# Kernel optimization log

Hardware: AMD Instinct MI355X
Metric: run time of the kernel (lower is better)

Reference implementation:

```python
import jax, jax.numpy as jnp
import numpy as np

BATCH = 1024
LATENT = 16
IMG = 3 * 96 * 96  # 27648


def setup_inputs() -> dict:
    key = jax.random.key(0)
    ks = jax.random.split(key, 16)
    w = lambda k, shape, s=0.05: (jax.random.normal(k, shape, jnp.float32) * s)
    return {
        "x": jax.random.normal(ks[0], (BATCH, 96, 96, 3), jnp.float32),
        "eps_noise": jax.random.normal(ks[1], (BATCH, LATENT), jnp.float32),
        "enc_w1": w(ks[2], (IMG, 900)),
        "enc_b1": jnp.zeros((900,), jnp.float32),
        "enc_w2": w(ks[3], (900, 300)),
        "enc_b2": jnp.zeros((300,), jnp.float32),
        "logvar_w": w(ks[4], (300, LATENT)),
        "logvar_b": jnp.zeros((LATENT,), jnp.float32),
        "W": w(ks[5], (LATENT, LATENT), 0.1),  # nn.init.normal_(std=0.1)
        "dec_w1": w(ks[6], (LATENT, 300)),
        "dec_b1": jnp.zeros((300,), jnp.float32),
        "dec_w2": w(ks[7], (300, 300)),
        "dec_b2": jnp.zeros((300,), jnp.float32),
        "dec_w3": w(ks[8], (300, IMG)),
        "dec_b3": jnp.zeros((IMG,), jnp.float32),
    }


def reference(x, eps_noise, enc_w1, enc_b1, enc_w2, enc_b2, logvar_w, logvar_b,
              W, dec_w1, dec_b1, dec_w2, dec_b2, dec_w3, dec_b3):
    # encoder
    xf = x.reshape(x.shape[0], -1)                      # [B, 27648]
    h = jax.nn.elu(xf @ enc_w1 + enc_b1)
    h = jax.nn.elu(h @ enc_w2 + enc_b2)
    logvar = h @ logvar_w + logvar_b                    # [B, d]

    d = W.shape[0]
    idx = jnp.arange(d, dtype=W.dtype)
    relu_y = jnp.maximum(idx[None, :] - idx[:, None], 0.0)  # ReLU(j - i), strictly upper tri
    Bmat = W * relu_y                                    # strictly upper triangular

    # latent generating process: z_j = sum_{i<j} z_i B[i,j] + eps_j  <=>  z (I - B) = eps
    eps = jnp.exp(logvar / 2.0) * eps_noise             # [B, d]
    A = jnp.eye(d, dtype=W.dtype) - Bmat                # upper triangular
    # solve A^T z^T = eps^T (forward substitution), one fused triangular solve
    z = jax.scipy.linalg.solve_triangular(A, eps.T, trans=1, lower=False).T
    Bz = z @ Bmat                                       # equals per-column z[:, :j] @ B[:j, j]

    # decoder
    g = jax.nn.elu(z @ dec_w1 + dec_b1)
    g = jax.nn.elu(g @ dec_w2 + dec_b2)
    xhat = jnp.tanh(g @ dec_w3 + dec_b3).reshape(-1, 96, 96, 3)
    return z, logvar, Bz, Bmat, xhat
```

## Files before the change

kernel.cpp:

```cpp
#include <hip/hip_runtime.h>
#include <math.h>

#define ACT_NONE 0
#define ACT_ELU  1
#define ACT_TANH 2

typedef unsigned short u16;
typedef unsigned int   u32;
typedef __attribute__((ext_vector_type(8))) short short8;
typedef __attribute__((ext_vector_type(4))) float f32x4;

__device__ __forceinline__ float eluf(float v) { return v > 0.f ? v : __expf(v) - 1.f; }
__device__ __forceinline__ float tanh_fast(float v) {
    float t = __expf(2.f * v);
    return 1.f - 2.f / (t + 1.f);
}
__device__ __forceinline__ u16 bf16_rne(float x) {
    u32 u = __float_as_uint(x);
    u32 r = u + 0x7FFFu + ((u >> 16) & 1u);
    return (u16)(r >> 16);
}

__global__ __launch_bounds__(256) void splitX(
    const float* __restrict__ in, u16* __restrict__ hi, u16* __restrict__ lo, int n)
{
    int i = (blockIdx.x * 256 + threadIdx.x) * 8;
    if (i >= n) return;
    float4 v0 = reinterpret_cast<const float4*>(in + i)[0];
    float4 v1 = reinterpret_cast<const float4*>(in + i)[1];
    float f[8] = {v0.x, v0.y, v0.z, v0.w, v1.x, v1.y, v1.z, v1.w};
    alignas(16) u16 h[8], l[8];
#pragma unroll
    for (int e = 0; e < 8; ++e) {
        u16 hh = bf16_rne(f[e]);
        h[e] = hh;
        float hf = __uint_as_float((u32)hh << 16);
        l[e] = bf16_rne(f[e] - hf);
    }
    *reinterpret_cast<uint4*>(hi + i) = *reinterpret_cast<uint4*>(&h[0]);
    *reinterpret_cast<uint4*>(lo + i) = *reinterpret_cast<uint4*>(&l[0]);
}

__global__ __launch_bounds__(256) void convT(
    const float* __restrict__ in, int K, int N,
    u16* __restrict__ outHi, u16* __restrict__ outLo, int ldo)
{
    __shared__ float tile[32][33];
    const int t  = threadIdx.x;
    const int kt = blockIdx.x * 32;
    const int nt = blockIdx.y * 32;
    {
        int r = t >> 3, c = (t & 7) * 4;
        int gk = kt + r;
        float4 v = {0.f, 0.f, 0.f, 0.f};
        if (gk < K) {
            const float* p = in + (size_t)gk * N + nt + c;
            if (nt + c + 3 < N) {
                v = *reinterpret_cast<const float4*>(p);
            } else {
                if (nt + c + 0 < N) v.x = p[0];
                if (nt + c + 1 < N) v.y = p[1];
                if (nt + c + 2 < N) v.z = p[2];
                if (nt + c + 3 < N) v.w = p[3];
            }
        }
        tile[r][c] = v.x; tile[r][c + 1] = v.y; tile[r][c + 2] = v.z; tile[r][c + 3] = v.w;
    }
    __syncthreads();
    {
        int r = t >> 3, c = (t & 7) * 4;
        ushort4 h, l;
        float f[4];
#pragma unroll
        for (int e = 0; e < 4; ++e) f[e] = tile[c + e][r];
        u16 hh[4], ll[4];
#pragma unroll
        for (int e = 0; e < 4; ++e) {
            hh[e] = bf16_rne(f[e]);
            float hf = __uint_as_float((u32)hh[e] << 16);
            ll[e] = bf16_rne(f[e] - hf);
        }
        h.x = hh[0]; h.y = hh[1]; h.z = hh[2]; h.w = hh[3];
        l.x = ll[0]; l.y = ll[1]; l.z = ll[2]; l.w = ll[3];
        size_t o = (size_t)(nt + r) * ldo + kt + c;
        *reinterpret_cast<ushort4*>(outHi + o) = h;
        *reinterpret_cast<ushort4*>(outLo + o) = l;
    }
}

template <int ACT, bool ATOMIC>
__global__ __launch_bounds__(256) void mgemm2(
    const u16* __restrict__ Ahi, const u16* __restrict__ Alo, int lda,
    const u16* __restrict__ Bhi, const u16* __restrict__ Blo, int ldb,
    const float* __restrict__ bias,
    float* __restrict__ C, int ldc,
    int Ncols, int kChunk, int Ktot)
{
    __shared__ u16 As[2][128][40];
    __shared__ u16 Bs[2][128][40];

    const int tid  = threadIdx.x;
    const int m0   = blockIdx.y * 128;
    const int n0   = blockIdx.x * 128;
    const int kbeg = blockIdx.z * kChunk;
    const int kend = min(Ktot, kbeg + kChunk);

    const int w  = tid >> 6;
    const int wm = (w >> 1) * 64;
    const int wn = (w & 1) * 64;
    const int ln = tid & 63;
    const int fr = ln & 15;
    const int kh = ln >> 4;

    const int srow = tid >> 1;
    const int skq  = (tid & 1) * 16;

    const u16* pAh = Ahi + (size_t)(m0 + srow) * lda + skq;
    const u16* pAl = Alo + (size_t)(m0 + srow) * lda + skq;
    const u16* pBh = Bhi + (size_t)(n0 + srow) * ldb + skq;
    const u16* pBl = Blo + (size_t)(n0 + srow) * ldb + skq;

    uint4 r0, r1, r2, r3, r4, r5, r6, r7;
#define LOADK(kk) do {                                                   \
        r0 = *reinterpret_cast<const uint4*>(pAh + (kk));                \
        r1 = *reinterpret_cast<const uint4*>(pAh + (kk) + 8);            \
        r2 = *reinterpret_cast<const uint4*>(pAl + (kk));                \
        r3 = *reinterpret_cast<const uint4*>(pAl + (kk) + 8);            \
        r4 = *reinterpret_cast<const uint4*>(pBh + (kk));                \
        r5 = *reinterpret_cast<const uint4*>(pBh + (kk) + 8);            \
        r6 = *reinterpret_cast<const uint4*>(pBl + (kk));                \
        r7 = *reinterpret_cast<const uint4*>(pBl + (kk) + 8);            \
    } while (0)

    f32x4 acc[4][4];
#pragma unroll
    for (int i = 0; i < 4; ++i)
#pragma unroll
        for (int j = 0; j < 4; ++j) {
            f32x4 z = {0.f, 0.f, 0.f, 0.f};
            acc[i][j] = z;
        }

    LOADK(kbeg);
    for (int k0 = kbeg; k0 < kend; k0 += 32) {
        *reinterpret_cast<uint4*>(&As[0][srow][skq])     = r0;
        *reinterpret_cast<uint4*>(&As[0][srow][skq + 8]) = r1;
        *reinterpret_cast<uint4*>(&As[1][srow][skq])     = r2;
        *reinterpret_cast<uint4*>(&As[1][srow][skq + 8]) = r3;
        *reinterpret_cast<uint4*>(&Bs[0][srow][skq])     = r4;
        *reinterpret_cast<uint4*>(&Bs[0][srow][skq + 8]) = r5;
        *reinterpret_cast<uint4*>(&Bs[1][srow][skq])     = r6;
        *reinterpret_cast<uint4*>(&Bs[1][srow][skq + 8]) = r7;
        __syncthreads();

        if (k0 + 32 < kend) LOADK(k0 + 32);

        short8 ah[4], al[4], bh[4], bl[4];
#pragma unroll
        for (int i = 0; i < 4; ++i) {
            ah[i] = *reinterpret_cast<const short8*>(&As[0][wm + i * 16 + fr][kh * 8]);
            al[i] = *reinterpret_cast<const short8*>(&As[1][wm + i * 16 + fr][kh * 8]);
        }
#pragma unroll
        for (int j = 0; j < 4; ++j) {
            bh[j] = *reinterpret_cast<const short8*>(&Bs[0][wn + j * 16 + fr][kh * 8]);
            bl[j] = *reinterpret_cast<const short8*>(&Bs[1][wn + j * 16 + fr][kh * 8]);
        }
#pragma unroll
        for (int i = 0; i < 4; ++i)
#pragma unroll
            for (int j = 0; j < 4; ++j) {
                acc[i][j] = __builtin_amdgcn_mfma_f32_16x16x32_bf16(ah[i], bh[j], acc[i][j], 0, 0, 0);
                acc[i][j] = __builtin_amdgcn_mfma_f32_16x16x32_bf16(ah[i], bl[j], acc[i][j], 0, 0, 0);
                acc[i][j] = __builtin_amdgcn_mfma_f32_16x16x32_bf16(al[i], bh[j], acc[i][j], 0, 0, 0);
            }
        __syncthreads();
    }
#undef LOADK

#pragma unroll
    for (int j = 0; j < 4; ++j) {
        const int col = n0 + wn + j * 16 + fr;
        float bv = 0.f;
        if (!ATOMIC) bv = bias[col];
#pragma unroll
        for (int i = 0; i < 4; ++i) {
            const int rowb = m0 + wm + i * 16 + kh * 4;
#pragma unroll
            for (int p = 0; p < 4; ++p) {
                float v = acc[i][j][p];
                const int row = rowb + p;
                if (ATOMIC) {
                    if (col < Ncols) atomicAdd(&C[(size_t)row * ldc + col], v);
                } else {
                    v += bv;
                    if (ACT == ACT_TANH) v = tanh_fast(v);
                    else if (ACT == ACT_ELU) v = eluf(v);
                    C[(size_t)row * ldc + col] = v;
                }
            }
        }
    }
}

__global__ __launch_bounds__(256) void zero_f32(float* __restrict__ p, int n)
{
    int i = blockIdx.x * 256 + threadIdx.x;
    if (i < n) p[i] = 0.f;
}

__global__ __launch_bounds__(256) void bias_elu_inplace(
    float* __restrict__ p, const float* __restrict__ bias, int n, int N)
{
    int i = blockIdx.x * 256 + threadIdx.x;
    if (i < n) p[i] = eluf(p[i] + bias[i % N]);
}

template <int ACT>
__global__ __launch_bounds__(256) void rowgemm(
    const float* __restrict__ A, int strideA,
    const float* __restrict__ W, const float* __restrict__ bias,
    float* __restrict__ out, int strideOut, int padWidth,
    int N, int K)
{
    __shared__ float Arow[928];
    const int m = blockIdx.x;
    const int t = threadIdx.x;
    for (int k = t; k < K; k += 256) Arow[k] = A[(size_t)m * strideA + k];
    __syncthreads();
    for (int n = t; n < padWidth; n += 256) {
        float s = 0.f;
        if (n < N) {
            s = bias[n];
            for (int k = 0; k < K; ++k) s = fmaf(Arow[k], W[(size_t)k * N + n], s);
            if (ACT == ACT_ELU) s = eluf(s);
        }
        out[(size_t)m * strideOut + n] = s;
    }
}

__global__ __launch_bounds__(256) void rowgemm_split(
    const float* __restrict__ A, int strideA,
    const float* __restrict__ W, const float* __restrict__ bias,
    u16* __restrict__ outHi, u16* __restrict__ outLo, int strideOut, int padWidth,
    int N, int K)
{
    __shared__ float Arow[928];
    const int m = blockIdx.x;
    const int t = threadIdx.x;
    for (int k = t; k < K; k += 256) Arow[k] = A[(size_t)m * strideA + k];
    __syncthreads();
    for (int n = t; n < padWidth; n += 256) {
        u16 hh = 0, ll = 0;
        if (n < N) {
            float s = bias[n];
            for (int k = 0; k < K; ++k) s = fmaf(Arow[k], W[(size_t)k * N + n], s);
            s = eluf(s);
            hh = bf16_rne(s);
            float hf = __uint_as_float((u32)hh << 16);
            ll = bf16_rne(s - hf);
        }
        outHi[(size_t)m * strideOut + n] = hh;
        outLo[(size_t)m * strideOut + n] = ll;
    }
}

__global__ __launch_bounds__(256) void latent_kernel(
    const float* __restrict__ logvar,
    const float* __restrict__ eps_noise,
    const float* __restrict__ Wlat,
    float* __restrict__ z_ws,
    float* __restrict__ out)
{
    __shared__ float Bm[256];
    const int t = threadIdx.x;
    {
        int i = t >> 4, j = t & 15;
        float v = (j > i) ? Wlat[t] * (float)(j - i) : 0.f;
        Bm[t] = v;
        if (blockIdx.x == 0) out[49152 + t] = v;
    }
    __syncthreads();

    const int b = blockIdx.x * 256 + t;
    float lv[16], z[16];
#pragma unroll
    for (int j = 0; j < 16; ++j) lv[j] = logvar[b * 16 + j];
#pragma unroll
    for (int j = 0; j < 16; ++j) {
        float s = __expf(0.5f * fminf(lv[j], 80.f)) * eps_noise[b * 16 + j];
        for (int i = 0; i < j; ++i) s = fmaf(z[i], Bm[i * 16 + j], s);
        z[j] = s;
    }
#pragma unroll
    for (int j = 0; j < 16; ++j) {
        float bz = 0.f;
#pragma unroll
        for (int i = 0; i < 16; ++i) bz = fmaf(z[i], Bm[i * 16 + j], bz);
        out[b * 16 + j]         = z[j];
        out[16384 + b * 16 + j] = lv[j];
        out[32768 + b * 16 + j] = bz;
        z_ws[b * 16 + j] = z[j];
    }
}

extern "C" void kernel_launch(void* const* d_in, const int* in_sizes, int n_in,
                              void* d_out, int out_size, void* d_ws, size_t ws_size,
                              hipStream_t stream)
{
    const float* x       = (const float*)d_in[0];
    const float* eps_n   = (const float*)d_in[1];
    const float* enc_w1  = (const float*)d_in[2];
    const float* enc_b1  = (const float*)d_in[3];
    const float* enc_w2  = (const float*)d_in[4];
    const float* enc_b2  = (const float*)d_in[5];
    const float* lv_w    = (const float*)d_in[6];
    const float* lv_b    = (const float*)d_in[7];
    const float* Wlat    = (const float*)d_in[8];
    const float* dec_w1  = (const float*)d_in[9];
    const float* dec_b1  = (const float*)d_in[10];
    const float* dec_w2  = (const float*)d_in[11];
    const float* dec_b2  = (const float*)d_in[12];
    const float* dec_w3  = (const float*)d_in[13];
    const float* dec_b3  = (const float*)d_in[14];

    char* ws = (char*)d_ws;
    float* h1     = (float*)(ws + 0);
    float* h2     = (float*)(ws + 3686400);
    float* lv     = (float*)(ws + 4915200);
    float* zf     = (float*)(ws + 4980736);
    float* g1     = (float*)(ws + 5046272);
    u16*   g2hi   = (u16*)(ws + 6275072);
    u16*   g2lo   = (u16*)(ws + 6930432);
    u16*   xhi    = (u16*)(ws + 7585792);
    u16*   xlo    = (u16*)(ws + 64208896);
    u16*   w1t_hi = (u16*)(ws + 120832000);
    u16*   w1t_lo = (u16*)(ws + 177455104);
    u16*   w3t_hi = (u16*)(ws + 234078208);
    u16*   w3t_lo = (u16*)(ws + 251772928);

    float* out = (float*)d_out;

    splitX<<<13824, 256, 0, stream>>>(x, xhi, xlo, 28311552);

    convT<<<dim3(864, 32), 256, 0, stream>>>(enc_w1, 27648, 900, w1t_hi, w1t_lo, 27648);
    convT<<<dim3(10, 864), 256, 0, stream>>>(dec_w3, 300, 27648, w3t_hi, w3t_lo, 320);

    zero_f32<<<3600, 256, 0, stream>>>(h1, 921600);

    mgemm2<ACT_NONE, true><<<dim3(8, 8, 16), 256, 0, stream>>>(
        xhi, xlo, 27648, w1t_hi, w1t_lo, 27648, nullptr,
        h1, 900, 900, 1728, 27648);

    bias_elu_inplace<<<3600, 256, 0, stream>>>(h1, enc_b1, 921600, 900);

    rowgemm<ACT_ELU><<<1024, 256, 0, stream>>>(
        h1, 900, enc_w2, enc_b2, h2, 300, 300, 300, 900);

    rowgemm<ACT_NONE><<<1024, 256, 0, stream>>>(
        h2, 300, lv_w, lv_b, lv, 16, 16, 16, 300);

    latent_kernel<<<4, 256, 0, stream>>>(lv, eps_n, Wlat, zf, out);

    rowgemm<ACT_ELU><<<1024, 256, 0, stream>>>(
        zf, 16, dec_w1, dec_b1, g1, 300, 300, 300, 16);

    rowgemm_split<<<1024, 256, 0, stream>>>(
        g1, 300, dec_w2, dec_b2, g2hi, g2lo, 320, 320, 300, 300);

    mgemm2<ACT_TANH, false><<<dim3(216, 8, 1), 256, 0, stream>>>(
        g2hi, g2lo, 320, w3t_hi, w3t_lo, 320, dec_b3,
        out + 49408, 27648, 27648, 320, 320);
}
```

Measured before the change: 969.7 us.

## Fuse X bf16 split into encoder GEMM and replace atomics with split-K partials

The encoder GEMM now reads fp32 x directly and splits it into bf16 hi/lo inside the load stage, dropping the separate splitX pass and its large hi/lo intermediate buffers. Split-K results go to per-slice partial buffers instead of being atomically added into a pre-zeroed buffer. A vectorized reduce kernel then sums the partials and applies bias and ELU. Block indices are also remapped into a swizzled 1D grid to improve cache locality across compute units. The cost is extra conversion ALU inside the GEMM and a partial-buffer write and read pass.

```diff
diff --git a/kernel.cpp b/kernel.cpp
--- a/kernel.cpp
+++ b/kernel.cpp
@@ -19,26 +19,6 @@
     u32 u = __float_as_uint(x);
     u32 r = u + 0x7FFFu + ((u >> 16) & 1u);
     return (u16)(r >> 16);
-}
-
-__global__ __launch_bounds__(256) void splitX(
-    const float* __restrict__ in, u16* __restrict__ hi, u16* __restrict__ lo, int n)
-{
-    int i = (blockIdx.x * 256 + threadIdx.x) * 8;
-    if (i >= n) return;
-    float4 v0 = reinterpret_cast<const float4*>(in + i)[0];
-    float4 v1 = reinterpret_cast<const float4*>(in + i)[1];
-    float f[8] = {v0.x, v0.y, v0.z, v0.w, v1.x, v1.y, v1.z, v1.w};
-    alignas(16) u16 h[8], l[8];
-#pragma unroll
-    for (int e = 0; e < 8; ++e) {
-        u16 hh = bf16_rne(f[e]);
-        h[e] = hh;
-        float hf = __uint_as_float((u32)hh << 16);
-        l[e] = bf16_rne(f[e] - hf);
-    }
-    *reinterpret_cast<uint4*>(hi + i) = *reinterpret_cast<uint4*>(&h[0]);
-    *reinterpret_cast<uint4*>(lo + i) = *reinterpret_cast<uint4*>(&l[0]);
 }
 
 __global__ __launch_bounds__(256) void convT(
@@ -88,21 +68,29 @@
     }
 }
 
-template <int ACT, bool ATOMIC>
-__global__ __launch_bounds__(256) void mgemm2(
+template <int ACT, bool AFP32, bool PARTIAL>
+__global__ __launch_bounds__(256) void mgemm3(
+    const float* __restrict__ Af,
     const u16* __restrict__ Ahi, const u16* __restrict__ Alo, int lda,
     const u16* __restrict__ Bhi, const u16* __restrict__ Blo, int ldb,
     const float* __restrict__ bias,
-    float* __restrict__ C, int ldc,
-    int Ncols, int kChunk, int Ktot)
+    float* __restrict__ C, int ldc, int partStride,
+    int Ncols, int kChunk, int Ktot, int nTiles, int mTiles)
 {
     __shared__ u16 As[2][128][40];
     __shared__ u16 Bs[2][128][40];
 
+    const int cpx = gridDim.x >> 3;
+    const int lid = (blockIdx.x & 7) * cpx + (blockIdx.x >> 3);
+    const int nT  = lid % nTiles;
+    const int rem = lid / nTiles;
+    const int mT  = rem % mTiles;
+    const int z   = rem / mTiles;
+
     const int tid  = threadIdx.x;
-    const int m0   = blockIdx.y * 128;
-    const int n0   = blockIdx.x * 128;
-    const int kbeg = blockIdx.z * kChunk;
+    const int m0   = mT * 128;
+    const int n0   = nT * 128;
+    const int kbeg = z * kChunk;
     const int kend = min(Ktot, kbeg + kChunk);
 
     const int w  = tid >> 6;
@@ -115,38 +103,69 @@
     const int srow = tid >> 1;
     const int skq  = (tid & 1) * 16;
 
-    const u16* pAh = Ahi + (size_t)(m0 + srow) * lda + skq;
-    const u16* pAl = Alo + (size_t)(m0 + srow) * lda + skq;
-    const u16* pBh = Bhi + (size_t)(n0 + srow) * ldb + skq;
-    const u16* pBl = Blo + (size_t)(n0 + srow) * ldb + skq;
-
-    uint4 r0, r1, r2, r3, r4, r5, r6, r7;
-#define LOADK(kk) do {                                                   \
-        r0 = *reinterpret_cast<const uint4*>(pAh + (kk));                \
-        r1 = *reinterpret_cast<const uint4*>(pAh + (kk) + 8);            \
-        r2 = *reinterpret_cast<const uint4*>(pAl + (kk));                \
-        r3 = *reinterpret_cast<const uint4*>(pAl + (kk) + 8);            \
-        r4 = *reinterpret_cast<const uint4*>(pBh + (kk));                \
-        r5 = *reinterpret_cast<const uint4*>(pBh + (kk) + 8);            \
-        r6 = *reinterpret_cast<const uint4*>(pBl + (kk));                \
-        r7 = *reinterpret_cast<const uint4*>(pBl + (kk) + 8);            \
-    } while (0)
+    const float* pAf = AFP32 ? (Af + (size_t)(m0 + srow) * lda + skq) : nullptr;
+    const u16*   pAh = AFP32 ? nullptr : (Ahi + (size_t)(m0 + srow) * lda + skq);
+    const u16*   pAl = AFP32 ? nullptr : (Alo + (size_t)(m0 + srow) * lda + skq);
+    const u16*   pBh = Bhi + (size_t)(n0 + srow) * ldb + skq;
+    const u16*   pBl = Blo + (size_t)(n0 + srow) * ldb + skq;
+
+    float4 fa0, fa1, fa2, fa3;
+    uint4  r0, r1, r2, r3;
+    uint4  r4, r5, r6, r7;
+
+    auto LOADK = [&](int kk) {
+        if constexpr (AFP32) {
+            fa0 = reinterpret_cast<const float4*>(pAf + kk)[0];
+            fa1 = reinterpret_cast<const float4*>(pAf + kk)[1];
+            fa2 = reinterpret_cast<const float4*>(pAf + kk)[2];
+            fa3 = reinterpret_cast<const float4*>(pAf + kk)[3];
+        } else {
+            r0 = *reinterpret_cast<const uint4*>(pAh + kk);
+            r1 = *reinterpret_cast<const uint4*>(pAh + kk + 8);
+            r2 = *reinterpret_cast<const uint4*>(pAl + kk);
+            r3 = *reinterpret_cast<const uint4*>(pAl + kk + 8);
+        }
+        r4 = *reinterpret_cast<const uint4*>(pBh + kk);
+        r5 = *reinterpret_cast<const uint4*>(pBh + kk + 8);
+        r6 = *reinterpret_cast<const uint4*>(pBl + kk);
+        r7 = *reinterpret_cast<const uint4*>(pBl + kk + 8);
+    };
 
     f32x4 acc[4][4];
 #pragma unroll
     for (int i = 0; i < 4; ++i)
 #pragma unroll
         for (int j = 0; j < 4; ++j) {
-            f32x4 z = {0.f, 0.f, 0.f, 0.f};
-            acc[i][j] = z;
+            f32x4 zz = {0.f, 0.f, 0.f, 0.f};
+            acc[i][j] = zz;
         }
 
     LOADK(kbeg);
     for (int k0 = kbeg; k0 < kend; k0 += 32) {
-        *reinterpret_cast<uint4*>(&As[0][srow][skq])     = r0;
-        *reinterpret_cast<uint4*>(&As[0][srow][skq + 8]) = r1;
-        *reinterpret_cast<uint4*>(&As[1][srow][skq])     = r2;
-        *reinterpret_cast<uint4*>(&As[1][srow][skq + 8]) = r3;
+        if constexpr (AFP32) {
+            alignas(16) float vv[16];
+            *reinterpret_cast<float4*>(&vv[0])  = fa0;
+            *reinterpret_cast<float4*>(&vv[4])  = fa1;
+            *reinterpret_cast<float4*>(&vv[8])  = fa2;
+            *reinterpret_cast<float4*>(&vv[12]) = fa3;
+            alignas(16) u16 hh[16], ll[16];
+#pragma unroll
+            for (int e = 0; e < 16; ++e) {
+                u16 h = bf16_rne(vv[e]);
+                hh[e] = h;
+                float hf = __uint_as_float((u32)h << 16);
+                ll[e] = bf16_rne(vv[e] - hf);
+            }
+            *reinterpret_cast<uint4*>(&As[0][srow][skq])     = *reinterpret_cast<uint4*>(&hh[0]);
+            *reinterpret_cast<uint4*>(&As[0][srow][skq + 8]) = *reinterpret_cast<uint4*>(&hh[8]);
+            *reinterpret_cast<uint4*>(&As[1][srow][skq])     = *reinterpret_cast<uint4*>(&ll[0]);
+            *reinterpret_cast<uint4*>(&As[1][srow][skq + 8]) = *reinterpret_cast<uint4*>(&ll[8]);
+        } else {
+            *reinterpret_cast<uint4*>(&As[0][srow][skq])     = r0;
+            *reinterpret_cast<uint4*>(&As[0][srow][skq + 8]) = r1;
+            *reinterpret_cast<uint4*>(&As[1][srow][skq])     = r2;
+            *reinterpret_cast<uint4*>(&As[1][srow][skq + 8]) = r3;
+        }
         *reinterpret_cast<uint4*>(&Bs[0][srow][skq])     = r4;
         *reinterpret_cast<uint4*>(&Bs[0][srow][skq + 8]) = r5;
         *reinterpret_cast<uint4*>(&Bs[1][srow][skq])     = r6;
@@ -176,13 +195,13 @@
             }
         __syncthreads();
     }
-#undef LOADK
-
+
+    float* Cz = PARTIAL ? (C + (size_t)z * partStride) : C;
 #pragma unroll
     for (int j = 0; j < 4; ++j) {
         const int col = n0 + wn + j * 16 + fr;
         float bv = 0.f;
-        if (!ATOMIC) bv = bias[col];
+        if (!PARTIAL) bv = bias[col];
 #pragma unroll
         for (int i = 0; i < 4; ++i) {
             const int rowb = m0 + wm + i * 16 + kh * 4;
@@ -190,30 +209,35 @@
             for (int p = 0; p < 4; ++p) {
                 float v = acc[i][j][p];
                 const int row = rowb + p;
-                if (ATOMIC) {
-                    if (col < Ncols) atomicAdd(&C[(size_t)row * ldc + col], v);
+                if (PARTIAL) {
+                    if (col < Ncols) Cz[(size_t)row * ldc + col] = v;
                 } else {
                     v += bv;
                     if (ACT == ACT_TANH) v = tanh_fast(v);
                     else if (ACT == ACT_ELU) v = eluf(v);
-                    C[(size_t)row * ldc + col] = v;
+                    Cz[(size_t)row * ldc + col] = v;
                 }
             }
         }
     }
 }
 
-__global__ __launch_bounds__(256) void zero_f32(float* __restrict__ p, int n)
-{
-    int i = blockIdx.x * 256 + threadIdx.x;
-    if (i < n) p[i] = 0.f;
-}
-
-__global__ __launch_bounds__(256) void bias_elu_inplace(
-    float* __restrict__ p, const float* __restrict__ bias, int n, int N)
-{
-    int i = blockIdx.x * 256 + threadIdx.x;
-    if (i < n) p[i] = eluf(p[i] + bias[i % N]);
+__global__ __launch_bounds__(256) void reduce_bias_elu(
+    const float* __restrict__ part, const float* __restrict__ bias,
+    float* __restrict__ out, int n, int N, int nz, int partStride)
+{
+    int i = (blockIdx.x * 256 + threadIdx.x) * 4;
+    if (i >= n) return;
+    float4 s = *reinterpret_cast<const float4*>(part + i);
+    for (int z = 1; z < nz; ++z) {
+        float4 p = *reinterpret_cast<const float4*>(part + (size_t)z * partStride + i);
+        s.x += p.x; s.y += p.y; s.z += p.z; s.w += p.w;
+    }
+    int c = i % N;
+    float4 b = *reinterpret_cast<const float4*>(bias + c);
+    s.x = eluf(s.x + b.x); s.y = eluf(s.y + b.y);
+    s.z = eluf(s.z + b.z); s.w = eluf(s.w + b.w);
+    *reinterpret_cast<float4*>(out + i) = s;
 }
 
 template <int ACT>
@@ -325,34 +349,30 @@
     const float* dec_b3  = (const float*)d_in[14];
 
     char* ws = (char*)d_ws;
-    float* h1     = (float*)(ws + 0);
-    float* h2     = (float*)(ws + 3686400);
-    float* lv     = (float*)(ws + 4915200);
-    float* zf     = (float*)(ws + 4980736);
-    float* g1     = (float*)(ws + 5046272);
-    u16*   g2hi   = (u16*)(ws + 6275072);
-    u16*   g2lo   = (u16*)(ws + 6930432);
-    u16*   xhi    = (u16*)(ws + 7585792);
-    u16*   xlo    = (u16*)(ws + 64208896);
-    u16*   w1t_hi = (u16*)(ws + 120832000);
-    u16*   w1t_lo = (u16*)(ws + 177455104);
-    u16*   w3t_hi = (u16*)(ws + 234078208);
-    u16*   w3t_lo = (u16*)(ws + 251772928);
+    float* part   = (float*)(ws + 0);
+    float* h1     = (float*)(ws + 58982400);
+    float* h2     = (float*)(ws + 62668800);
+    float* lv     = (float*)(ws + 63897600);
+    float* zf     = (float*)(ws + 63963136);
+    float* g1     = (float*)(ws + 64028672);
+    u16*   g2hi   = (u16*)(ws + 65257472);
+    u16*   g2lo   = (u16*)(ws + 65912832);
+    u16*   w1t_hi = (u16*)(ws + 66568192);
+    u16*   w1t_lo = (u16*)(ws + 123191296);
+    u16*   w3t_hi = (u16*)(ws + 179814400);
+    u16*   w3t_lo = (u16*)(ws + 197509120);
 
     float* out = (float*)d_out;
-
-    splitX<<<13824, 256, 0, stream>>>(x, xhi, xlo, 28311552);
 
     convT<<<dim3(864, 32), 256, 0, stream>>>(enc_w1, 27648, 900, w1t_hi, w1t_lo, 27648);
     convT<<<dim3(10, 864), 256, 0, stream>>>(dec_w3, 300, 27648, w3t_hi, w3t_lo, 320);
 
-    zero_f32<<<3600, 256, 0, stream>>>(h1, 921600);
-
-    mgemm2<ACT_NONE, true><<<dim3(8, 8, 16), 256, 0, stream>>>(
-        xhi, xlo, 27648, w1t_hi, w1t_lo, 27648, nullptr,
-        h1, 900, 900, 1728, 27648);
-
-    bias_elu_inplace<<<3600, 256, 0, stream>>>(h1, enc_b1, 921600, 900);
+    mgemm3<ACT_NONE, true, true><<<1024, 256, 0, stream>>>(
+        x, nullptr, nullptr, 27648,
+        w1t_hi, w1t_lo, 27648, nullptr,
+        part, 900, 921600, 900, 1728, 27648, 8, 8);
+
+    reduce_bias_elu<<<900, 256, 0, stream>>>(part, enc_b1, h1, 921600, 900, 16, 921600);
 
     rowgemm<ACT_ELU><<<1024, 256, 0, stream>>>(
         h1, 900, enc_w2, enc_b2, h2, 300, 300, 300, 900);
@@ -368,7 +388,8 @@
     rowgemm_split<<<1024, 256, 0, stream>>>(
         g1, 300, dec_w2, dec_b2, g2hi, g2lo, 320, 320, 300, 300);
 
-    mgemm2<ACT_TANH, false><<<dim3(216, 8, 1), 256, 0, stream>>>(
-        g2hi, g2lo, 320, w3t_hi, w3t_lo, 320, dec_b3,
-        out + 49408, 27648, 27648, 320, 320);
-}
+    mgemm3<ACT_TANH, false, false><<<1728, 256, 0, stream>>>(
+        nullptr, g2hi, g2lo, 320,
+        w3t_hi, w3t_lo, 320, dec_b3,
+        out + 49408, 27648, 0, 27648, 320, 320, 216, 8);
+}
```

Measured after the change: 914.9 us. -5.7%, faster.
